# Optimization experiments

Hardware: AMD Instinct MI355X
Metric: run time of the kernel (lower is better)

The kernel has to match this reference:

```python
import jax, jax.numpy as jnp
import numpy as np
import math

B, L, D, H, FF = 2, 2048, 1024, 16, 4096
FACTOR = 5
EPS = 1e-5


def _ln(x, g, b):
    mu = jnp.mean(x, axis=-1, keepdims=True)
    var = jnp.mean((x - mu) ** 2, axis=-1, keepdims=True)
    return (x - mu) * jax.lax.rsqrt(var + EPS) * g + b


def setup_inputs() -> dict:
    key = jax.random.key(0)
    ks = jax.random.split(key, 16)
    s = D ** -0.5
    sample_k = min(FACTOR * int(np.ceil(np.log(L))), L)  # 40
    return {
        "x": jax.random.normal(ks[0], (B, L, D), jnp.float32),
        "Wq": jax.random.normal(ks[1], (D, D), jnp.float32) * s,
        "bq": jnp.zeros((D,), jnp.float32),
        "Wk": jax.random.normal(ks[2], (D, D), jnp.float32) * s,
        "bk": jnp.zeros((D,), jnp.float32),
        "Wv": jax.random.normal(ks[3], (D, D), jnp.float32) * s,
        "bv": jnp.zeros((D,), jnp.float32),
        "Wo": jax.random.normal(ks[4], (D, D), jnp.float32) * s,
        "bo": jnp.zeros((D,), jnp.float32),
        "ln1_g": jnp.ones((D,), jnp.float32),
        "ln1_b": jnp.zeros((D,), jnp.float32),
        "W1": jax.random.normal(ks[5], (D, FF), jnp.float32) * s,
        "b1": jnp.zeros((FF,), jnp.float32),
        "W2": jax.random.normal(ks[6], (FF, D), jnp.float32) * (FF ** -0.5),
        "b2": jnp.zeros((D,), jnp.float32),
        "ln2_g": jnp.ones((D,), jnp.float32),
        "ln2_b": jnp.zeros((D,), jnp.float32),
        "index_sample": jax.random.randint(ks[7], (L, sample_k), 0, L),
    }


def _prob_attn(Q, K, V, index_sample):
    # Q,K,V: [B,H,L,Dh]; Informer ProbAttention with mask_flag=True (causal).
    b, h, l, dh = Q.shape
    n_top = min(FACTOR * int(np.ceil(np.log(l))), l)
    # sampled scores: Q[l] . K[index_sample[l, s]]
    K_s = K[:, :, index_sample]                                  # [B,H,L,S,Dh]
    QKs = jnp.einsum("bhld,bhlsd->bhls", Q, K_s)                 # [B,H,L,S]
    M = QKs.max(-1) - QKs.sum(-1) / l                             # sparsity measure
    _, M_top = jax.lax.top_k(M, n_top)                            # [B,H,u]
    Q_red = jnp.take_along_axis(Q, M_top[..., None], axis=2)      # [B,H,u,Dh]
    scale = 1.0 / jnp.sqrt(jnp.asarray(dh, jnp.float32))
    scores = jnp.einsum("bhud,bhld->bhul", Q_red, K) * scale      # [B,H,u,L]
    causal = jnp.arange(l)[None, None, None, :] > M_top[..., None]
    scores = jnp.where(causal, -jnp.inf, scores)
    attn = jax.nn.softmax(scores, axis=-1)
    upd = jnp.einsum("bhul,bhld->bhud", attn, V)                  # [B,H,u,Dh]
    # initial context for masked case: running cumsum of V
    context = jnp.cumsum(V, axis=2)
    bi = jnp.arange(b)[:, None, None]
    hi = jnp.arange(h)[None, :, None]
    context = context.at[bi, hi, M_top].set(upd)
    return context                                               # [B,H,L,Dh]


def reference(x, Wq, bq, Wk, bk, Wv, bv, Wo, bo, ln1_g, ln1_b,
              W1, b1, W2, b2, ln2_g, ln2_b, index_sample):
    b, l, d = x.shape
    dh = d // H
    Q = (x @ Wq + bq).reshape(b, l, H, dh).transpose(0, 2, 1, 3)
    K = (x @ Wk + bk).reshape(b, l, H, dh).transpose(0, 2, 1, 3)
    V = (x @ Wv + bv).reshape(b, l, H, dh).transpose(0, 2, 1, 3)
    ctx = _prob_attn(Q, K, V, index_sample)
    ctx = ctx.transpose(0, 2, 1, 3).reshape(b, l, d)
    attn_out = ctx @ Wo + bo
    x1 = _ln(x + attn_out, ln1_g, ln1_b)
    ff = jnp.maximum(x1 @ W1 + b1, 0.0) @ W2 + b2
    return _ln(x1 + ff, ln2_g, ln2_b)
```

## Files before the change

### kernel.cpp

```cpp
#include <hip/hip_runtime.h>
#include <hip/hip_bf16.h>
#include <hip/hip_fp16.h>
#include <math.h>

constexpr int B = 2, L = 2048, D = 1024, H = 16, DH = 64, FFD = 4096;
constexpr int S = 40;
constexpr int U = 40;
constexpr float EPS = 1e-5f;
constexpr int NCHUNK = 32;
constexpr int CHLEN = L / NCHUNK;
constexpr int LD3 = 3 * D;
constexpr int LD2 = 2 * D;
constexpr int LDA2 = 2 * D;
constexpr int JT = 128;
constexpr int NJC = L / JT;

typedef __attribute__((ext_vector_type(8))) short short8;
typedef __attribute__((ext_vector_type(8))) _Float16 half8;
typedef __attribute__((ext_vector_type(4))) float f32x4;

__device__ __forceinline__ unsigned short f2bf(float v) {
  __hip_bfloat16 h = __float2bfloat16(v);
  return __builtin_bit_cast(unsigned short, h);
}
__device__ __forceinline__ float bf2f(unsigned short u) {
  unsigned int x = ((unsigned int)u) << 16;
  return __builtin_bit_cast(float, x);
}
__device__ __forceinline__ unsigned short f2h(float v) {
  __half h = __float2half(v);
  return __builtin_bit_cast(unsigned short, h);
}
__device__ __forceinline__ float h2f(unsigned short u) {
  return __half2float(__builtin_bit_cast(__half, u));
}

__device__ __forceinline__ void gload16(const void* g, void* l) {
  __builtin_amdgcn_global_load_lds(
      (const __attribute__((address_space(1))) void*)g,
      (__attribute__((address_space(3))) void*)l, 16, 0, 0);
}

template<int GBN, int MINB, bool RELU, bool OUT_BF16, bool F16, bool DUPA>
__global__ __launch_bounds__(256, MINB) void gemm_kernel(
    const unsigned short* __restrict__ A,
    const unsigned short* __restrict__ Bt,
    const float* __restrict__ bias,
    const float* __restrict__ biasB,
    void* __restrict__ C, int M, int N, int K, int KA) {
  constexpr int GBM = 128, GBK = 64;
  constexpr int ABUF = GBM * GBK;
  constexpr int BBUF = GBN * GBK;
  constexpr int BUFS = ABUF + BBUF;
  constexpr int NI = GBN / 32;
  constexpr int NLOADS = 4 + GBN / 32;
  __shared__ short lds[2 * BUFS];

  const int tid  = threadIdx.x;
  const int lane = tid & 63;
  const int wid  = tid >> 6;
  const int wr = wid >> 1;
  const int wc = wid & 1;

  const int nwg  = gridDim.x * gridDim.y;
  const int orig = blockIdx.y * gridDim.x + blockIdx.x;
  const int wg   = (orig & 7) * (nwg >> 3) + (orig >> 3);
  const int bm = (wg / gridDim.x) * GBM;
  const int bn = (wg % gridDim.x) * GBN;

  const int srow  = lane >> 3;
  const int sslot = (lane & 7) ^ srow;
  const unsigned short* aS = A  + (size_t)(bm + wid * 8 + srow) * KA + sslot * 8;
  const unsigned short* bS = Bt + (size_t)(bn + wid * 8 + srow) * K  + sslot * 8;
  short* la0 = lds + wid * 8 * GBK;
  short* lb0 = lds + ABUF + wid * 8 * GBK;

  auto STAGE = [&](int buf, int kt) {
    const int akt = (DUPA && kt >= 16) ? kt - 16 : kt;
    const unsigned short* ap = aS + (size_t)akt * GBK;
    const unsigned short* bp = bS + (size_t)kt  * GBK;
    short* la = la0 + buf * BUFS;
    short* lb = lb0 + buf * BUFS;
    gload16(ap,                   la);
    gload16(ap + (size_t)32 * KA, la + 32 * GBK);
    gload16(ap + (size_t)64 * KA, la + 64 * GBK);
    gload16(ap + (size_t)96 * KA, la + 96 * GBK);
    #pragma unroll
    for (int r = 0; r < GBN / 32; ++r)
      gload16(bp + (size_t)(r * 32) * K, lb + r * 32 * GBK);
  };

  const int fr = lane & 15, g = lane >> 4;
  const int nt = K / GBK;

  STAGE(0, 0);

  f32x4 acc[4][NI] = {};
  int cur = 0;
  for (int t = 0; t < nt; ++t) {
    const int kt = (t + 1 < nt) ? t + 1 : t;
    STAGE(cur ^ 1, kt);
    if constexpr (NLOADS == 8)
      asm volatile("s_waitcnt vmcnt(8)" ::: "memory");
    else
      asm volatile("s_waitcnt vmcnt(6)" ::: "memory");
    __builtin_amdgcn_sched_barrier(0);
    __builtin_amdgcn_s_barrier();

    const short* la = lds + cur * BUFS;
    const short* lb = la + ABUF;
    short8 av[2][4], bv[2][NI];
    #pragma unroll
    for (int kk = 0; kk < 2; ++kk) {
      #pragma unroll
      for (int mi = 0; mi < 4; ++mi) {
        const int row = wr * 64 + mi * 16 + fr;
        av[kk][mi] = *(const short8*)&la[row * GBK + ((((kk << 2) | g) ^ (fr & 7)) << 3)];
      }
      #pragma unroll
      for (int ni = 0; ni < NI; ++ni) {
        const int row = wc * (GBN / 2) + ni * 16 + fr;
        bv[kk][ni] = *(const short8*)&lb[row * GBK + ((((kk << 2) | g) ^ (fr & 7)) << 3)];
      }
    }
    __builtin_amdgcn_s_setprio(1);
    #pragma unroll
    for (int kk = 0; kk < 2; ++kk)
      #pragma unroll
      for (int mi = 0; mi < 4; ++mi)
        #pragma unroll
        for (int ni = 0; ni < NI; ++ni) {
          if constexpr (F16)
            acc[mi][ni] = __builtin_amdgcn_mfma_f32_16x16x32_f16(
                __builtin_bit_cast(half8, av[kk][mi]),
                __builtin_bit_cast(half8, bv[kk][ni]), acc[mi][ni], 0, 0, 0);
          else
            acc[mi][ni] = __builtin_amdgcn_mfma_f32_16x16x32_bf16(
                av[kk][mi], bv[kk][ni], acc[mi][ni], 0, 0, 0);
        }
    __builtin_amdgcn_s_setprio(0);
    asm volatile("s_waitcnt lgkmcnt(0)" ::: "memory");
    __builtin_amdgcn_sched_barrier(0);
    __builtin_amdgcn_s_barrier();
    cur ^= 1;
  }

  #pragma unroll
  for (int ni = 0; ni < NI; ++ni) {
    const int col = bn + wc * (GBN / 2) + ni * 16 + fr;
    const float bcol = DUPA ? (col < D ? bias[col] : biasB[col - D]) : bias[col];
    #pragma unroll
    for (int mi = 0; mi < 4; ++mi) {
      #pragma unroll
      for (int j = 0; j < 4; ++j) {
        const int rowg = bm + wr * 64 + mi * 16 + (g << 2) + j;
        float v = acc[mi][ni][j] + bcol;
        if (RELU) v = fmaxf(v, 0.f);
        if (OUT_BF16) ((unsigned short*)C)[(size_t)rowg * N + col] = f2bf(v);
        else          ((float*)C)[(size_t)rowg * N + col] = v;
      }
    }
  }
}

__global__ __launch_bounds__(256) void prep_kernel(
    const float* __restrict__ x, unsigned short* __restrict__ A2,
    unsigned short* __restrict__ xb,
    const float* __restrict__ Wq, const float* __restrict__ Wk,
    unsigned short* __restrict__ B2r,
    const float* __restrict__ Wv, const float* __restrict__ Wo,
    const float* __restrict__ W1, const float* __restrict__ W2,
    unsigned short* __restrict__ Wvt, unsigned short* __restrict__ Wot,
    unsigned short* __restrict__ W1t, unsigned short* __restrict__ W2t) {
  const int bid = blockIdx.x;
  __shared__ float tile[32][33];
  if (bid < 4096) {
    const int i = (bid * 256 + threadIdx.x) * 4;
    const int m = i / D, k = i % D;
    const float4 v = *(const float4*)(x + i);
    ushort4 hi, lo, bb;
    hi.x = f2h(v.x); lo.x = f2h(v.x - h2f(hi.x)); bb.x = f2bf(v.x);
    hi.y = f2h(v.y); lo.y = f2h(v.y - h2f(hi.y)); bb.y = f2bf(v.y);
    hi.z = f2h(v.z); lo.z = f2h(v.z - h2f(hi.z)); bb.z = f2bf(v.z);
    hi.w = f2h(v.w); lo.w = f2h(v.w - h2f(hi.w)); bb.w = f2bf(v.w);
    unsigned short* row = A2 + (size_t)m * LDA2;
    *(ushort4*)(row + k)     = hi;
    *(ushort4*)(row + D + k) = lo;
    *(ushort4*)(xb + i) = bb;
    return;
  }
  const int tx = threadIdx.x & 31, ty = threadIdx.x >> 5;
  if (bid < 6144) {
    const int t = bid - 4096;
    const int z = t >> 10;
    const float* W = z ? Wk : Wq;
    unsigned short* outb = B2r + (size_t)z * D * LD3;
    const int bx = ((t & 1023) & 31) * 32;
    const int by = ((t & 1023) >> 5) * 32;
    #pragma unroll
    for (int i = ty; i < 32; i += 8)
      tile[i][tx] = W[(size_t)(by + i) * D + bx + tx];
    __syncthreads();
    #pragma unroll
    for (int i = ty; i < 32; i += 8) {
      const float v = tile[tx][i];
      const unsigned short hi = f2h(v);
      const unsigned short lo = f2h(v - h2f(hi));
      unsigned short* r = outb + (size_t)(bx + i) * LD3 + (by + tx);
      r[0]     = hi;
      r[D]     = lo;
      r[2 * D] = hi;
    }
    return;
  }
  const int tb = bid - 6144;
  const float* W; unsigned short* Wt; int K, N, t;
  if (tb < 1024)      { W = Wv; Wt = Wvt; K = D;   N = D;   t = tb; }
  else if (tb < 2048) { W = Wo; Wt = Wot; K = D;   N = D;   t = tb - 1024; }
  else if (tb < 6144) { W = W1; Wt = W1t; K = D;   N = FFD; t = tb - 2048; }
  else                { W = W2; Wt = W2t; K = FFD; N = D;   t = tb - 6144; }
  const int nx = N / 32;
  const int bx = (t % nx) * 32;
  const int by = (t / nx) * 32;
  #pragma unroll
  for (int i = ty; i < 32; i += 8)
    tile[i][tx] = W[(size_t)(by + i) * N + bx + tx];
  __syncthreads();
  #pragma unroll
  for (int i = ty; i < 32; i += 8)
    Wt[(size_t)(bx + i) * K + by + tx] = f2bf(tile[tx][i]);
}

__global__ __launch_bounds__(256) void prob_m_kernel(
    const float* __restrict__ QK, const int* __restrict__ idx,
    float* __restrict__ M_) {
  const int combo = blockIdx.x;
  const int b = combo >> 2, hg = combo & 3;
  const int l = blockIdx.y;
  const int tid = threadIdx.x;
  const int wave = tid >> 6;
  const int lane = tid & 63;
  const int h = hg * 4 + wave;
  __shared__ int sidx[S];
  if (tid < S) sidx[tid] = idx[l * S + tid];
  __syncthreads();
  const int dsub = (lane & 15) * 4;
  const int sgrp = lane >> 4;
  const float4 q = *(const float4*)(QK + ((size_t)b * L + l) * LD2 + h * DH + dsub);
  float mx = -INFINITY, sm = 0.f;
  for (int s = sgrp; s < S; s += 4) {
    const float4 kv = *(const float4*)(QK + ((size_t)b * L + sidx[s]) * LD2 + D + h * DH + dsub);
    float p = q.x*kv.x + q.y*kv.y + q.z*kv.z + q.w*kv.w;
    p += __shfl_xor(p, 1);
    p += __shfl_xor(p, 2);
    p += __shfl_xor(p, 4);
    p += __shfl_xor(p, 8);
    mx = fmaxf(mx, p);
    sm += p;
  }
  mx = fmaxf(mx, __shfl_xor(mx, 16));
  mx = fmaxf(mx, __shfl_xor(mx, 32));
  sm += __shfl_xor(sm, 16);
  sm += __shfl_xor(sm, 32);
  if (lane == 0)
    M_[((size_t)b * H + h) * L + l] = mx - sm / (float)L;
}

__global__ __launch_bounds__(64) void topk_kernel(
    const float* __restrict__ M_, int* __restrict__ Mtop) {
  const int bh = blockIdx.x;
  const float* row = M_ + (size_t)bh * L;
  const int lane = threadIdx.x;
  float v[32];
  #pragma unroll
  for (int k = 0; k < 32; ++k) v[k] = row[k * 64 + lane];
  for (int u = 0; u < U; ++u) {
    float best = v[0]; int bk = 0;
    #pragma unroll
    for (int k = 1; k < 32; ++k)
      if (v[k] > best) { best = v[k]; bk = k; }
    int bidx = bk * 64 + lane;
    #pragma unroll
    for (int off = 1; off < 64; off <<= 1) {
      const float ov = __shfl_xor(best, off);
      const int   oi = __shfl_xor(bidx, off);
      if (ov > best || (ov == best && oi < bidx)) { best = ov; bidx = oi; }
    }
    if (lane == 0) Mtop[bh * U + u] = bidx;
    if ((bidx & 63) == lane) {
      const int kk = bidx >> 6;
      #pragma unroll
      for (int k = 0; k < 32; ++k) if (k == kk) v[k] = -INFINITY;
    }
  }
}

__global__ __launch_bounds__(320) void attn_p1_kernel(
    const float* __restrict__ QK, const unsigned short* __restrict__ V16,
    const int* __restrict__ Mtop,
    float* __restrict__ pmax, float* __restrict__ psum, float* __restrict__ pv) {
  const int jc = blockIdx.x, h = blockIdx.y, b = blockIdx.z;
  const int bh = b * H + h;
  const int tid = threadIdx.x;
  const int j0 = jc * JT;
  __shared__ float Qs[U][68];
  __shared__ float KVs[JT][68];
  __shared__ unsigned short ws[U][JT];

  for (int i = tid; i < U * 16; i += 320) {
    const int u = i >> 4, dq = (i & 15) << 2;
    const int row = Mtop[bh * U + u];
    *(float4*)&Qs[u][dq] =
        *(const float4*)(QK + ((size_t)b * L + row) * LD2 + h * DH + dq);
  }
  for (int i = tid; i < JT * 16; i += 320) {
    const int j = i >> 4, dq = (i & 15) << 2;
    *(float4*)&KVs[j][dq] =
        *(const float4*)(QK + ((size_t)b * L + j0 + j) * LD2 + D + h * DH + dq);
  }
  __syncthreads();

  const int u = tid >> 3, jg = tid & 7;
  const int mt = Mtop[bh * U + u];
  float sc[16];
  #pragma unroll
  for (int jt = 0; jt < 16; ++jt) sc[jt] = 0.f;
  for (int dq = 0; dq < 64; dq += 4) {
    const float4 q = *(const float4*)&Qs[u][dq];
    #pragma unroll
    for (int jt = 0; jt < 16; ++jt) {
      const float4 k = *(const float4*)&KVs[jt * 8 + jg][dq];
      sc[jt] += q.x*k.x + q.y*k.y + q.z*k.z + q.w*k.w;
    }
  }
  float m = -INFINITY;
  #pragma unroll
  for (int jt = 0; jt < 16; ++jt) {
    const int j = j0 + jt * 8 + jg;
    sc[jt] = (j <= mt) ? sc[jt] * 0.125f : -INFINITY;
    m = fmaxf(m, sc[jt]);
  }
  m = fmaxf(m, __shfl_xor(m, 1));
  m = fmaxf(m, __shfl_xor(m, 2));
  m = fmaxf(m, __shfl_xor(m, 4));
  float sum = 0.f;
  #pragma unroll
  for (int jt = 0; jt < 16; ++jt) {
    const float e = (sc[jt] == -INFINITY) ? 0.f : expf(sc[jt] - m);
    sum += e;
    ws[u][jt * 8 + jg] = f2bf(e);
  }
  sum += __shfl_xor(sum, 1);
  sum += __shfl_xor(sum, 2);
  sum += __shfl_xor(sum, 4);
  if (jg == 0) {
    pmax[(size_t)(bh * NJC + jc) * U + u] = m;
    psum[(size_t)(bh * NJC + jc) * U + u] = sum;
  }
  __syncthreads();
  for (int i = tid; i < JT * 8; i += 320) {
    const int j = i >> 3, d8 = (i & 7) << 3;
    short8 vv = *(const short8*)(V16 + ((size_t)b * L + j0 + j) * D + h * DH + d8);
    #pragma unroll
    for (int e = 0; e < 8; ++e)
      KVs[j][d8 + e] = bf2f((unsigned short)vv[e]);
  }
  __syncthreads();
  const int d = tid & 63, ug = tid >> 6;
  float acc[8] = {};
  for (int j = 0; j < JT; j += 2) {
    const float v0 = KVs[j][d], v1 = KVs[j + 1][d];
    #pragma unroll
    for (int k = 0; k < 8; ++k) {
      const int uu = ug + k * 5;
      const unsigned int wp = *(const unsigned int*)&ws[uu][j];
      acc[k] = fmaf(bf2f((unsigned short)(wp & 0xffff)), v0, acc[k]);
      acc[k] = fmaf(bf2f((unsigned short)(wp >> 16)), v1, acc[k]);
    }
  }
  #pragma unroll
  for (int k = 0; k < 8; ++k) {
    const int uu = ug + k * 5;
    pv[((size_t)(bh * NJC + jc) * U + uu) * DH + d] = acc[k];
  }
}

__global__ __launch_bounds__(64) void attn_p2_kernel(
    const float* __restrict__ pmax, const float* __restrict__ psum,
    const float* __restrict__ pv, const int* __restrict__ Mtop,
    unsigned short* __restrict__ ctx16) {
  const int bid = blockIdx.x;
  const int u = bid % U, bh = bid / U;
  const int d = threadIdx.x;
  float gmax = -INFINITY;
  for (int c = 0; c < NJC; ++c)
    gmax = fmaxf(gmax, pmax[(size_t)(bh * NJC + c) * U + u]);
  float den = 0.f, num = 0.f;
  for (int c = 0; c < NJC; ++c) {
    const float m = pmax[(size_t)(bh * NJC + c) * U + u];
    if (m == -INFINITY) continue;
    const float s = expf(m - gmax);
    den += psum[(size_t)(bh * NJC + c) * U + u] * s;
    num += pv[((size_t)(bh * NJC + c) * U + u) * DH + d] * s;
  }
  const int h = bh % H, b = bh / H;
  const int l = Mtop[bh * U + u];
  ctx16[((size_t)b * L + l) * D + h * DH + d] = f2bf(num / den);
}

__global__ __launch_bounds__(256) void cumsum_pass1(
    const unsigned short* __restrict__ V16, float* __restrict__ csums) {
  const int cp = blockIdx.x * 256 + threadIdx.x;
  const int ch = blockIdx.y, b = blockIdx.z;
  size_t base = ((size_t)b * L + (size_t)ch * CHLEN) * D + cp * 2;
  float a0 = 0.f, a1 = 0.f;
  for (int i = 0; i < CHLEN; ++i) {
    const unsigned int u = *(const unsigned int*)(V16 + base + (size_t)i * D);
    a0 += bf2f((unsigned short)(u & 0xffff));
    a1 += bf2f((unsigned short)(u >> 16));
  }
  float* cs = csums + ((size_t)b * NCHUNK + ch) * D + cp * 2;
  cs[0] = a0; cs[1] = a1;
}

__global__ __launch_bounds__(256) void cumsum_pass2(
    const unsigned short* __restrict__ V16, const float* __restrict__ csums,
    unsigned short* __restrict__ ctx16) {
  const int cp = blockIdx.x * 256 + threadIdx.x;
  const int ch = blockIdx.y, b = blockIdx.z;
  float a0 = 0.f, a1 = 0.f;
  for (int j = 0; j < ch; ++j) {
    const float* cs = csums + ((size_t)b * NCHUNK + j) * D + cp * 2;
    a0 += cs[0]; a1 += cs[1];
  }
  size_t base = ((size_t)b * L + (size_t)ch * CHLEN) * D + cp * 2;
  for (int i = 0; i < CHLEN; ++i) {
    const size_t o = base + (size_t)i * D;
    const unsigned int u = *(const unsigned int*)(V16 + o);
    a0 += bf2f((unsigned short)(u & 0xffff));
    a1 += bf2f((unsigned short)(u >> 16));
    *(unsigned int*)(ctx16 + o) =
        (unsigned int)f2bf(a0) | ((unsigned int)f2bf(a1) << 16);
  }
}

template<bool ABF16>
__global__ __launch_bounds__(256) void add_ln_kernel(
    const void* __restrict__ a_, const unsigned short* __restrict__ r,
    const float* __restrict__ g, const float* __restrict__ be,
    float* __restrict__ out, unsigned short* __restrict__ out16) {
  const int row = blockIdx.x;
  const int tid = threadIdx.x;
  __shared__ float buf[D];
  __shared__ float red[256];
  float s = 0.f;
  for (int i = tid; i < D; i += 256) {
    float av;
    if (ABF16) av = bf2f(((const unsigned short*)a_)[(size_t)row * D + i]);
    else       av = ((const float*)a_)[(size_t)row * D + i];
    float v = av + bf2f(r[(size_t)row * D + i]);
    buf[i] = v; s += v;
  }
  red[tid] = s; __syncthreads();
  for (int off = 128; off > 0; off >>= 1) {
    if (tid < off) red[tid] += red[tid+off];
    __syncthreads();
  }
  const float mu = red[0] / (float)D;
  __syncthreads();
  float s2 = 0.f;
  for (int i = tid; i < D; i += 256) { float dv = buf[i] - mu; s2 += dv * dv; }
  red[tid] = s2; __syncthreads();
  for (int off = 128; off > 0; off >>= 1) {
    if (tid < off) red[tid] += red[tid+off];
    __syncthreads();
  }
  const float rstd = rsqrtf(red[0] / (float)D + EPS);
  __syncthreads();
  for (int i = tid; i < D; i += 256) {
    float v = (buf[i] - mu) * rstd * g[i] + be[i];
    if (out)   out[(size_t)row * D + i] = v;
    if (out16) out16[(size_t)row * D + i] = f2bf(v);
  }
}

extern "C" void kernel_launch(void* const* d_in, const int* in_sizes, int n_in,
                              void* d_out, int out_size, void* d_ws, size_t ws_size,
                              hipStream_t stream) {
  const float* x   = (const float*)d_in[0];
  const float* Wq  = (const float*)d_in[1];
  const float* bq  = (const float*)d_in[2];
  const float* Wk  = (const float*)d_in[3];
  const float* bk  = (const float*)d_in[4];
  const float* Wv  = (const float*)d_in[5];
  const float* bv  = (const float*)d_in[6];
  const float* Wo  = (const float*)d_in[7];
  const float* bo  = (const float*)d_in[8];
  const float* g1  = (const float*)d_in[9];
  const float* be1 = (const float*)d_in[10];
  const float* W1  = (const float*)d_in[11];
  const float* b1  = (const float*)d_in[12];
  const float* W2  = (const float*)d_in[13];
  const float* b2  = (const float*)d_in[14];
  const float* g2  = (const float*)d_in[15];
  const float* be2 = (const float*)d_in[16];
  const int*   idx = (const int*)d_in[17];
  float* out = (float*)d_out;

  char* p = (char*)d_ws;
  unsigned short* A2     = (unsigned short*)p;
  unsigned short* AO16   = (unsigned short*)p;
  unsigned short* ff2_16 = (unsigned short*)(p + 8388608);
  unsigned short* xb    = (unsigned short*)(p + 16777216);
  unsigned short* ctx16 = (unsigned short*)(p + 16777216);
  unsigned short* B2 = (unsigned short*)(p + 25165824);
  char* scr = p + 25165824;
  float* Mbuf   = (float*)(scr);
  float* csum   = (float*)(scr + 262144);
  int*   Mtop   = (int*)  (scr + 524288);
  float* pmax   = (float*)(scr + 532480);
  float* psum   = (float*)(scr + 614400);
  float* pv     = (float*)(scr + 696320);
  float*          QKb = (float*)(p + 37748736);
  unsigned short* x1b = (unsigned short*)(p + 54525952);
  unsigned short* ff1b = (unsigned short*)(p + 62914560);
  unsigned short* Vb16 = (unsigned short*)(p + 96468992);
  unsigned short* Wvt = (unsigned short*)(p + 113246208);
  unsigned short* Wot = (unsigned short*)(p + 115343360);
  unsigned short* W1t = (unsigned short*)(p + 117440512);
  unsigned short* W2t = (unsigned short*)(p + 125829120);

  dim3 blk(256);
  const int M = B * L;

  prep_kernel<<<16384, blk, 0, stream>>>(x, A2, xb, Wq, Wk, B2,
                                         Wv, Wo, W1, W2, Wvt, Wot, W1t, W2t);
  gemm_kernel<128,2,false,false,true,true><<<dim3(LD2/128, M/128), blk, 0, stream>>>(
      A2, B2, bq, bk, QKb, M, LD2, LD3, LDA2);
  gemm_kernel<64,3,false,true,false,false><<<dim3(D/64, M/128), blk, 0, stream>>>(
      xb, Wvt, bv, bv, Vb16, M, D, D, D);
  prob_m_kernel<<<dim3(8, L), blk, 0, stream>>>(QKb, idx, Mbuf);
  topk_kernel<<<B*H, dim3(64), 0, stream>>>(Mbuf, Mtop);
  attn_p1_kernel<<<dim3(NJC, H, B), dim3(320), 0, stream>>>(QKb, Vb16, Mtop, pmax, psum, pv);
  cumsum_pass1<<<dim3(D/512, NCHUNK, B), blk, 0, stream>>>(Vb16, csum);
  cumsum_pass2<<<dim3(D/512, NCHUNK, B), blk, 0, stream>>>(Vb16, csum, ctx16);
  attn_p2_kernel<<<B*H*U, dim3(64), 0, stream>>>(pmax, psum, pv, Mtop, ctx16);
  gemm_kernel<64,3,false,true,false,false><<<dim3(D/64, M/128), blk, 0, stream>>>(
      ctx16, Wot, bo, bo, AO16, M, D, D, D);
  add_ln_kernel<false><<<B*L, blk, 0, stream>>>(x, AO16, g1, be1, nullptr, x1b);
  gemm_kernel<128,2,true,true,false,false><<<dim3(FFD/128, M/128), blk, 0, stream>>>(
      x1b, W1t, b1, b1, ff1b, M, FFD, D, D);
  gemm_kernel<64,3,false,true,false,false><<<dim3(D/64, M/128), blk, 0, stream>>>(
      ff1b, W2t, b2, b2, ff2_16, M, D, FFD, FFD);
  add_ln_kernel<true><<<B*L, blk, 0, stream>>>(x1b, ff2_16, g2, be2, out,
                                               (unsigned short*)nullptr);
}
```

Baseline: 344.7 us.

## Add 256x256 eight-wave FF1 GEMM and warp-per-row LayerNorm

Replaces the FF1 GEMM with a dedicated 512-thread kernel that computes 256x256 tiles. It uses double-buffered swizzled LDS, interleaves global prefetch with MFMA phases under priority hints, and remaps workgroup IDs for locality. Separately, the add+LayerNorm kernel now handles one row per wavefront with vectorized loads and shuffle reductions, removing the shared-memory tree reductions and block barriers. The large tile gives more reuse per loaded byte but runs one block per CU and uses many registers.

```diff
diff --git a/kernel.cpp b/kernel.cpp
--- a/kernel.cpp
+++ b/kernel.cpp
@@ -158,6 +158,167 @@
         if (RELU) v = fmaxf(v, 0.f);
         if (OUT_BF16) ((unsigned short*)C)[(size_t)rowg * N + col] = f2bf(v);
         else          ((float*)C)[(size_t)rowg * N + col] = v;
+      }
+    }
+  }
+}
+
+__global__ __launch_bounds__(512, 1) void gemm_ff1_8ph_kernel(
+    const unsigned short* __restrict__ A,
+    const unsigned short* __restrict__ Bt,
+    const float* __restrict__ bias,
+    unsigned short* __restrict__ C, int M, int N, int K) {
+  constexpr int BK = 64;
+  __shared__ short lds8[2 * 32768];
+
+  const int tid  = threadIdx.x;
+  const int lane = tid & 63;
+  const int wid  = tid >> 6;
+  const int wrm  = wid >> 2;
+  const int wcn  = wid & 3;
+
+  const int nwg  = gridDim.x * gridDim.y;
+  const int orig = blockIdx.y * gridDim.x + blockIdx.x;
+  const int wg   = (orig & 7) * (nwg >> 3) + (orig >> 3);
+  const int bm = (wg / gridDim.x) * 256;
+  const int bn = (wg % gridDim.x) * 256;
+
+  const int srow  = lane >> 3;
+  const int sslot = (lane & 7) ^ srow;
+  const unsigned short* aS = A  + (size_t)(bm + wid * 8 + srow) * K + sslot * 8;
+  const unsigned short* bS = Bt + (size_t)(bn + wid * 8 + srow) * K + sslot * 8;
+  short* ldsA0 = lds8 + wid * 8 * BK;
+  short* ldsB0 = lds8 + 16384 + wid * 8 * BK;
+
+  auto STAGE2 = [&](int buf, int kt, int part) {
+    if (part < 2) {
+      const unsigned short* ap = aS + (size_t)kt * BK;
+      short* la = ldsA0 + buf * 32768;
+      const int r0 = part * 128;
+      gload16(ap + (size_t)r0 * K,        la + r0 * BK);
+      gload16(ap + (size_t)(r0 + 64) * K, la + (r0 + 64) * BK);
+    } else {
+      const unsigned short* bp = bS + (size_t)kt * BK;
+      short* lb = ldsB0 + buf * 32768;
+      const int r0 = (part - 2) * 128;
+      gload16(bp + (size_t)r0 * K,        lb + r0 * BK);
+      gload16(bp + (size_t)(r0 + 64) * K, lb + (r0 + 64) * BK);
+    }
+  };
+
+  const int fr = lane & 15, g = lane >> 4;
+  const int nt = K / BK;
+
+  #pragma unroll
+  for (int p = 0; p < 4; ++p) STAGE2(0, 0, p);
+
+  f32x4 acc[8][4] = {};
+  short8 av[2][4], bv0[2][2], bv1[2][2];
+  int bc = 0;
+  for (int t = 0; t < nt; ++t) {
+    const int kt = (t + 1 < nt) ? t + 1 : t;
+    const short* la = lds8 + bc * 32768;
+    const short* lb = la + 16384;
+
+    STAGE2(bc ^ 1, kt, 0);
+    asm volatile("s_waitcnt vmcnt(2)" ::: "memory");
+    __builtin_amdgcn_sched_barrier(0);
+    __builtin_amdgcn_s_barrier();
+
+    #pragma unroll
+    for (int kk = 0; kk < 2; ++kk) {
+      #pragma unroll
+      for (int mi = 0; mi < 4; ++mi) {
+        const int row = wrm * 128 + mi * 16 + fr;
+        av[kk][mi] = *(const short8*)&la[row * BK + ((((kk << 2) | g) ^ (fr & 7)) << 3)];
+      }
+      #pragma unroll
+      for (int ni = 0; ni < 2; ++ni) {
+        const int row = wcn * 64 + ni * 16 + fr;
+        bv0[kk][ni] = *(const short8*)&lb[row * BK + ((((kk << 2) | g) ^ (fr & 7)) << 3)];
+      }
+    }
+    asm volatile("s_waitcnt lgkmcnt(0)" ::: "memory");
+    __builtin_amdgcn_sched_barrier(0);
+    __builtin_amdgcn_s_setprio(1);
+    #pragma unroll
+    for (int kk = 0; kk < 2; ++kk)
+      #pragma unroll
+      for (int mi = 0; mi < 4; ++mi)
+        #pragma unroll
+        for (int ni = 0; ni < 2; ++ni)
+          acc[mi][ni] = __builtin_amdgcn_mfma_f32_16x16x32_bf16(
+              av[kk][mi], bv0[kk][ni], acc[mi][ni], 0, 0, 0);
+    __builtin_amdgcn_s_setprio(0);
+
+    STAGE2(bc ^ 1, kt, 1);
+    #pragma unroll
+    for (int kk = 0; kk < 2; ++kk)
+      #pragma unroll
+      for (int ni = 0; ni < 2; ++ni) {
+        const int row = wcn * 64 + 32 + ni * 16 + fr;
+        bv1[kk][ni] = *(const short8*)&lb[row * BK + ((((kk << 2) | g) ^ (fr & 7)) << 3)];
+      }
+    asm volatile("s_waitcnt lgkmcnt(0)" ::: "memory");
+    __builtin_amdgcn_sched_barrier(0);
+    __builtin_amdgcn_s_setprio(1);
+    #pragma unroll
+    for (int kk = 0; kk < 2; ++kk)
+      #pragma unroll
+      for (int mi = 0; mi < 4; ++mi)
+        #pragma unroll
+        for (int ni = 0; ni < 2; ++ni)
+          acc[mi][2 + ni] = __builtin_amdgcn_mfma_f32_16x16x32_bf16(
+              av[kk][mi], bv1[kk][ni], acc[mi][2 + ni], 0, 0, 0);
+    __builtin_amdgcn_s_setprio(0);
+
+    STAGE2(bc ^ 1, kt, 2);
+    #pragma unroll
+    for (int kk = 0; kk < 2; ++kk)
+      #pragma unroll
+      for (int mi = 0; mi < 4; ++mi) {
+        const int row = wrm * 128 + 64 + mi * 16 + fr;
+        av[kk][mi] = *(const short8*)&la[row * BK + ((((kk << 2) | g) ^ (fr & 7)) << 3)];
+      }
+    asm volatile("s_waitcnt lgkmcnt(0)" ::: "memory");
+    __builtin_amdgcn_sched_barrier(0);
+    __builtin_amdgcn_s_setprio(1);
+    #pragma unroll
+    for (int kk = 0; kk < 2; ++kk)
+      #pragma unroll
+      for (int mi = 0; mi < 4; ++mi)
+        #pragma unroll
+        for (int ni = 0; ni < 2; ++ni)
+          acc[4 + mi][ni] = __builtin_amdgcn_mfma_f32_16x16x32_bf16(
+              av[kk][mi], bv0[kk][ni], acc[4 + mi][ni], 0, 0, 0);
+    __builtin_amdgcn_s_setprio(0);
+
+    STAGE2(bc ^ 1, kt, 3);
+    __builtin_amdgcn_s_setprio(1);
+    #pragma unroll
+    for (int kk = 0; kk < 2; ++kk)
+      #pragma unroll
+      for (int mi = 0; mi < 4; ++mi)
+        #pragma unroll
+        for (int ni = 0; ni < 2; ++ni)
+          acc[4 + mi][2 + ni] = __builtin_amdgcn_mfma_f32_16x16x32_bf16(
+              av[kk][mi], bv1[kk][ni], acc[4 + mi][2 + ni], 0, 0, 0);
+    __builtin_amdgcn_s_setprio(0);
+    __builtin_amdgcn_s_barrier();
+    bc ^= 1;
+  }
+
+  #pragma unroll
+  for (int NJ = 0; NJ < 4; ++NJ) {
+    const int col = bn + wcn * 64 + NJ * 16 + fr;
+    const float bcol = bias[col];
+    #pragma unroll
+    for (int MI = 0; MI < 8; ++MI) {
+      #pragma unroll
+      for (int j = 0; j < 4; ++j) {
+        const int rowg = bm + wrm * 128 + MI * 16 + (g << 2) + j;
+        float v = fmaxf(acc[MI][NJ][j] + bcol, 0.f);
+        C[(size_t)rowg * N + col] = f2bf(v);
       }
     }
   }
@@ -449,38 +610,54 @@
     const void* __restrict__ a_, const unsigned short* __restrict__ r,
     const float* __restrict__ g, const float* __restrict__ be,
     float* __restrict__ out, unsigned short* __restrict__ out16) {
-  const int row = blockIdx.x;
-  const int tid = threadIdx.x;
-  __shared__ float buf[D];
-  __shared__ float red[256];
+  const int row  = blockIdx.x * 4 + (threadIdx.x >> 6);
+  const int lane = threadIdx.x & 63;
+  float v[16];
   float s = 0.f;
-  for (int i = tid; i < D; i += 256) {
-    float av;
-    if (ABF16) av = bf2f(((const unsigned short*)a_)[(size_t)row * D + i]);
-    else       av = ((const float*)a_)[(size_t)row * D + i];
-    float v = av + bf2f(r[(size_t)row * D + i]);
-    buf[i] = v; s += v;
-  }
-  red[tid] = s; __syncthreads();
-  for (int off = 128; off > 0; off >>= 1) {
-    if (tid < off) red[tid] += red[tid+off];
-    __syncthreads();
-  }
-  const float mu = red[0] / (float)D;
-  __syncthreads();
+  #pragma unroll
+  for (int j = 0; j < 4; ++j) {
+    const int c = j * 256 + lane * 4;
+    float4 av;
+    if (ABF16) {
+      ushort4 ua = *(const ushort4*)((const unsigned short*)a_ + (size_t)row * D + c);
+      av.x = bf2f(ua.x); av.y = bf2f(ua.y); av.z = bf2f(ua.z); av.w = bf2f(ua.w);
+    } else {
+      av = *(const float4*)((const float*)a_ + (size_t)row * D + c);
+    }
+    const ushort4 ur = *(const ushort4*)(r + (size_t)row * D + c);
+    v[j*4+0] = av.x + bf2f(ur.x);
+    v[j*4+1] = av.y + bf2f(ur.y);
+    v[j*4+2] = av.z + bf2f(ur.z);
+    v[j*4+3] = av.w + bf2f(ur.w);
+    s += v[j*4+0] + v[j*4+1] + v[j*4+2] + v[j*4+3];
+  }
+  #pragma unroll
+  for (int off = 1; off < 64; off <<= 1) s += __shfl_xor(s, off);
+  const float mu = s / (float)D;
   float s2 = 0.f;
-  for (int i = tid; i < D; i += 256) { float dv = buf[i] - mu; s2 += dv * dv; }
-  red[tid] = s2; __syncthreads();
-  for (int off = 128; off > 0; off >>= 1) {
-    if (tid < off) red[tid] += red[tid+off];
-    __syncthreads();
-  }
-  const float rstd = rsqrtf(red[0] / (float)D + EPS);
-  __syncthreads();
-  for (int i = tid; i < D; i += 256) {
-    float v = (buf[i] - mu) * rstd * g[i] + be[i];
-    if (out)   out[(size_t)row * D + i] = v;
-    if (out16) out16[(size_t)row * D + i] = f2bf(v);
+  #pragma unroll
+  for (int k = 0; k < 16; ++k) { const float dv = v[k] - mu; s2 += dv * dv; }
+  #pragma unroll
+  for (int off = 1; off < 64; off <<= 1) s2 += __shfl_xor(s2, off);
+  const float rstd = rsqrtf(s2 / (float)D + EPS);
+  #pragma unroll
+  for (int j = 0; j < 4; ++j) {
+    const int c = j * 256 + lane * 4;
+    const float4 gv = *(const float4*)(g + c);
+    const float4 bv = *(const float4*)(be + c);
+    float o0 = (v[j*4+0] - mu) * rstd * gv.x + bv.x;
+    float o1 = (v[j*4+1] - mu) * rstd * gv.y + bv.y;
+    float o2 = (v[j*4+2] - mu) * rstd * gv.z + bv.z;
+    float o3 = (v[j*4+3] - mu) * rstd * gv.w + bv.w;
+    if (out) {
+      float4 ov; ov.x = o0; ov.y = o1; ov.z = o2; ov.w = o3;
+      *(float4*)(out + (size_t)row * D + c) = ov;
+    }
+    if (out16) {
+      ushort4 uo;
+      uo.x = f2bf(o0); uo.y = f2bf(o1); uo.z = f2bf(o2); uo.w = f2bf(o3);
+      *(ushort4*)(out16 + (size_t)row * D + c) = uo;
+    }
   }
 }
 
@@ -547,11 +724,11 @@
   attn_p2_kernel<<<B*H*U, dim3(64), 0, stream>>>(pmax, psum, pv, Mtop, ctx16);
   gemm_kernel<64,3,false,true,false,false><<<dim3(D/64, M/128), blk, 0, stream>>>(
       ctx16, Wot, bo, bo, AO16, M, D, D, D);
-  add_ln_kernel<false><<<B*L, blk, 0, stream>>>(x, AO16, g1, be1, nullptr, x1b);
-  gemm_kernel<128,2,true,true,false,false><<<dim3(FFD/128, M/128), blk, 0, stream>>>(
-      x1b, W1t, b1, b1, ff1b, M, FFD, D, D);
+  add_ln_kernel<false><<<B*L/4, blk, 0, stream>>>(x, AO16, g1, be1, nullptr, x1b);
+  gemm_ff1_8ph_kernel<<<dim3(FFD/256, M/256), dim3(512), 0, stream>>>(
+      x1b, W1t, b1, ff1b, M, FFD, D);
   gemm_kernel<64,3,false,true,false,false><<<dim3(D/64, M/128), blk, 0, stream>>>(
       ff1b, W2t, b2, b2, ff2_16, M, D, FFD, FFD);
-  add_ln_kernel<true><<<B*L, blk, 0, stream>>>(x1b, ff2_16, g2, be2, out,
-                                               (unsigned short*)nullptr);
-}
+  add_ln_kernel<true><<<B*L/4, blk, 0, stream>>>(x1b, ff2_16, g2, be2, out,
+                                                 (unsigned short*)nullptr);
+}
```

Result: faster. 334.6 us, median of 2 (-2.9%).
